# Optimization experiments

Measured on AMD Instinct MI355X. Metric: run time of the kernel, lower is better.

The kernel has to match this reference:

```python
import jax, jax.numpy as jnp
import numpy as np

INPUT_DIM = 512
DEGREE = 3
NUM_KNOTS = 16
NUM_NEURONS = 1024
OUTPUT_DIM = 512
NUM_BASIS = NUM_KNOTS + DEGREE - 1  # 18


def make_knots():
    # uniform grid on [0,1], extended by `degree` knots on each side
    h = 1.0 / (NUM_KNOTS - 1)
    grid = np.linspace(0.0, 1.0, NUM_KNOTS)
    lo = grid[0] - h * np.arange(DEGREE, 0, -1)
    hi = grid[-1] + h * np.arange(1, DEGREE + 1)
    return jnp.asarray(np.concatenate([lo, grid, hi]), dtype=jnp.float32)  # [NUM_KNOTS+2*DEGREE]


def bspline_basis(x, t, degree):
    # x: [B, N]; t: [K] uniform extended knots. Cox-de Boor recursion.
    K = t.shape[0]
    xb = x[..., None]
    B = ((xb >= t[:-1]) & (xb < t[1:])).astype(x.dtype)  # [B, N, K-1]
    for p in range(1, degree + 1):
        ti = t[: K - p - 1]
        tip = t[p : K - 1]
        ti1 = t[1 : K - p]
        tip1 = t[p + 1 : K]
        left = (xb - ti) / (tip - ti) * B[..., :-1]
        right = (tip1 - xb) / (tip1 - ti1) * B[..., 1:]
        B = left + right
    return B  # [B, N, K-1-degree] == [B, N, NUM_BASIS]


def norm_layer(x, eps=1e-8):
    # per-row min-max normalization into the spline domain [0,1)
    mn = jnp.min(x, axis=-1, keepdims=True)
    mx = jnp.max(x, axis=-1, keepdims=True)
    return (x - mn) / (mx - mn + eps)


def setup_inputs() -> dict:
    key = jax.random.key(0)
    ks = jax.random.split(key, 7)
    x = jax.random.normal(ks[0], (4096, INPUT_DIM), dtype=jnp.float32)
    s1 = 1.0 / np.sqrt(INPUT_DIM)
    s2 = 1.0 / np.sqrt(NUM_NEURONS)
    W1 = jax.random.uniform(ks[1], (INPUT_DIM, NUM_NEURONS), jnp.float32, -s1, s1)
    b1 = jax.random.uniform(ks[2], (NUM_NEURONS,), jnp.float32, -s1, s1)
    coeff = jax.random.normal(ks[3], (NUM_NEURONS, NUM_BASIS), dtype=jnp.float32) * 0.1
    sp_bias = jnp.zeros((NUM_NEURONS,), dtype=jnp.float32)
    W2 = jax.random.uniform(ks[4], (NUM_NEURONS, OUTPUT_DIM), jnp.float32, -s2, s2)
    b2 = jax.random.uniform(ks[5], (OUTPUT_DIM,), jnp.float32, -s2, s2)
    return {"x": x, "W1": W1, "b1": b1, "coeff": coeff, "sp_bias": sp_bias, "W2": W2, "b2": b2}


def reference(x, W1, b1, coeff, sp_bias, W2, b2):
    t = make_knots()
    h = x @ W1 + b1                      # [B, N]  Linear 1
    h = norm_layer(h)                    # NormLayer -> [0,1)
    basis = bspline_basis(h, t, DEGREE)  # [B, N, NUM_BASIS]
    sp = jnp.einsum('bnk,nk->bn', basis, coeff) + sp_bias  # per-neuron spline eval
    out = sp @ W2 + b2                   # Linear 2
    return jax.nn.relu(out)
```

## Files before the change

kernel.cpp:

```cpp
#include <hip/hip_runtime.h>

#define M_ROWS  4096
#define IN_DIM  512
#define NEURONS 1024
#define OUT_DIM 512

typedef _Float16 f16;
typedef __attribute__((ext_vector_type(8))) _Float16 f16x8;
typedef __attribute__((ext_vector_type(4))) _Float16 f16x4;
typedef __attribute__((ext_vector_type(4))) float    f32x4;

__global__ __launch_bounds__(256) void prep(
    const float* __restrict__ x,  f16* __restrict__ xh,
    const float* __restrict__ W1, f16* __restrict__ W1t,
    const float* __restrict__ W2, f16* __restrict__ W2t,
    const float* __restrict__ coeff, const float* __restrict__ spb,
    f16* __restrict__ cpH)
{
    __shared__ float S[32][33];
    const int b = blockIdx.x, t = threadIdx.x;
    if (b < 1024) {
        int i = b * 256 + t;
        const float4* p = (const float4*)x;
        float4 a = p[i * 2], c = p[i * 2 + 1];
        f16x8 o = { (f16)a.x, (f16)a.y, (f16)a.z, (f16)a.w,
                    (f16)c.x, (f16)c.y, (f16)c.z, (f16)c.w };
        *(f16x8*)(xh + (size_t)i * 8) = o;
        return;
    }
    if (b < 1536) {
        const int tile = b - 1024;
        const int tx = tile & 31, ty = tile >> 5;
        const int tr = t >> 3, tc = (t & 7) * 4;
        float4 v = *(const float4*)&W1[(size_t)(ty * 32 + tr) * NEURONS + tx * 32 + tc];
        S[tr][tc + 0] = v.x; S[tr][tc + 1] = v.y;
        S[tr][tc + 2] = v.z; S[tr][tc + 3] = v.w;
        __syncthreads();
        f16x4 o = {(f16)S[tc + 0][tr], (f16)S[tc + 1][tr],
                   (f16)S[tc + 2][tr], (f16)S[tc + 3][tr]};
        *(f16x4*)&W1t[(size_t)(tx * 32 + tr) * IN_DIM + ty * 32 + tc] = o;
        return;
    }
    if (b < 2048) {
        const int tile = b - 1536;
        const int nt = tile & 15, kt2 = tile >> 4;
        const int tr = t >> 3, tc = (t & 7) * 4;
        float4 v = *(const float4*)&W2[(size_t)(kt2 * 32 + tr) * OUT_DIM + nt * 32 + tc];
        S[tr][tc + 0] = v.x; S[tr][tc + 1] = v.y;
        S[tr][tc + 2] = v.z; S[tr][tc + 3] = v.w;
        __syncthreads();
        const int n = nt * 32 + tr;
        f16x4 o = {(f16)S[tc + 0][tr], (f16)S[tc + 1][tr],
                   (f16)S[tc + 2][tr], (f16)S[tc + 3][tr]};
        const int kbyte = ((kt2 * 32 + tc) * 2) ^ ((n & 7) << 4);
        *(f16x4*)((char*)W2t + (size_t)n * 2048 + kbyte) = o;
        return;
    }
    {
        const int tid = (b - 2048) * 256 + t;
        if (tid < NEURONS * 15) {
            const int n = tid / 15, ii = tid % 15;
            const float s = spb[n];
            f16x4 c;
            c[0] = (f16)(coeff[n * 18 + ii]     + s);
            c[1] = (f16)(coeff[n * 18 + ii + 1] + s);
            c[2] = (f16)(coeff[n * 18 + ii + 2] + s);
            c[3] = (f16)(coeff[n * 18 + ii + 3] + s);
            *(f16x4*)&cpH[(size_t)tid * 4] = c;
        }
    }
}

__global__ __launch_bounds__(256) void k_gemm1(
    const f16* __restrict__ A, const f16* __restrict__ Bt,
    const float* __restrict__ b1, f16* __restrict__ h,
    float* __restrict__ pmin, float* __restrict__ pmax)
{
    __shared__ f16 lds[2][(128 + 64) * 64];

    const int t    = threadIdx.x;
    const int lane = t & 63, l15 = lane & 15, lhi = lane >> 4;
    const int wid  = t >> 6;
    const int wm   = wid >> 1, wn = wid & 1;

    const int flat = blockIdx.y * gridDim.x + blockIdx.x;
    const int swz  = (flat & 7) * 64 + (flat >> 3);
    const int m0   = (swz >> 4) * 128;
    const int n0   = (swz & 15) * 64;

    auto stage = [&](int buf, int kt) {
        f16* base = &lds[buf][0];
#pragma unroll
        for (int j = 0; j < 4; ++j) {
            int c = wid * 4 + j;
            const f16* g = A + (size_t)(m0 + c * 8 + (lane >> 3)) * IN_DIM + kt + (lane & 7) * 8;
            __builtin_amdgcn_global_load_lds(
                (const __attribute__((address_space(1))) void*)g,
                (__attribute__((address_space(3))) void*)(base + c * 512), 16, 0, 0);
        }
#pragma unroll
        for (int j = 0; j < 2; ++j) {
            int c = wid * 2 + j;
            const f16* g = Bt + (size_t)(n0 + c * 8 + (lane >> 3)) * IN_DIM + kt + (lane & 7) * 8;
            __builtin_amdgcn_global_load_lds(
                (const __attribute__((address_space(1))) void*)g,
                (__attribute__((address_space(3))) void*)(base + 8192 + c * 512), 16, 0, 0);
        }
    };

    f32x4 acc[4][2];
#pragma unroll
    for (int i = 0; i < 4; ++i)
#pragma unroll
        for (int j = 0; j < 2; ++j) acc[i][j] = (f32x4)0.f;

    stage(0, 0);
    __syncthreads();

    int cur = 0;
    for (int tt = 0; tt < 8; ++tt) {
        if (tt < 7) stage(cur ^ 1, (tt + 1) * 64);
        const f16* L = &lds[cur][0];
#pragma unroll
        for (int ks = 0; ks < 2; ++ks) {
            f16x8 bfr[2];
#pragma unroll
            for (int nj = 0; nj < 2; ++nj)
                bfr[nj] = *(const f16x8*)
                    &L[8192 + (wn * 32 + nj * 16 + l15) * 64 + ks * 32 + lhi * 8];
#pragma unroll
            for (int mi = 0; mi < 4; ++mi) {
                f16x8 afr = *(const f16x8*)
                    &L[(wm * 64 + mi * 16 + l15) * 64 + ks * 32 + lhi * 8];
#pragma unroll
                for (int nj = 0; nj < 2; ++nj)
                    acc[mi][nj] = __builtin_amdgcn_mfma_f32_16x16x32_f16(
                        afr, bfr[nj], acc[mi][nj], 0, 0, 0);
            }
        }
        __syncthreads();
        cur ^= 1;
    }

    const int nb2 = (n0 >> 6) * 2 + wn;
#pragma unroll
    for (int mi = 0; mi < 4; ++mi) {
        const int row0 = m0 + wm * 64 + mi * 16 + lhi * 4;
        float vmn[4], vmx[4];
#pragma unroll
        for (int nj = 0; nj < 2; ++nj) {
            const int col = n0 + wn * 32 + nj * 16 + l15;
            const float bv = b1[col];
#pragma unroll
            for (int j = 0; j < 4; ++j) {
                f16 hv = (f16)(acc[mi][nj][j] + bv);
                h[(size_t)(row0 + j) * NEURONS + col] = hv;
                float vr = (float)hv;
                if (nj == 0) { vmn[j] = vr; vmx[j] = vr; }
                else { vmn[j] = fminf(vmn[j], vr); vmx[j] = fmaxf(vmx[j], vr); }
            }
        }
#pragma unroll
        for (int j = 0; j < 4; ++j) {
#pragma unroll
            for (int d = 1; d < 16; d <<= 1) {
                vmn[j] = fminf(vmn[j], __shfl_xor(vmn[j], d));
                vmx[j] = fmaxf(vmx[j], __shfl_xor(vmx[j], d));
            }
        }
        if (l15 == 0) {
#pragma unroll
            for (int j = 0; j < 4; ++j) {
                pmin[(size_t)nb2 * M_ROWS + row0 + j] = vmn[j];
                pmax[(size_t)nb2 * M_ROWS + row0 + j] = vmx[j];
            }
        }
    }
}

__global__ __launch_bounds__(256) void sp_gemm2(
    const f16* __restrict__ h, const float* __restrict__ pmin,
    const float* __restrict__ pmax, const f16* __restrict__ cpH,
    const f16* __restrict__ W2t, const float* __restrict__ b2,
    float* __restrict__ out)
{
    __shared__ __align__(16) f16 Bb[2][128 * 64];
    __shared__ __align__(16) f16 Aa[2][32 * 72];
    __shared__ __align__(16) f16 cpS[2][4096];
    __shared__ float mnS[32], invS[32];

    const int t    = threadIdx.x;
    const int lane = t & 63, l15 = lane & 15, lhi = lane >> 4;
    const int wid  = t >> 6;
    const int wm   = wid & 1, wn = wid >> 1;

    const int flat = blockIdx.x;
    const int swz  = (flat & 7) * 64 + (flat >> 3);
    const int m0   = (swz & 127) * 32;
    const int n0   = (swz >> 7) * 128;

    auto stageB = [&](int s) {
        f16* base = &Bb[s & 1][0];
#pragma unroll
        for (int j = 0; j < 4; ++j) {
            const int c = wid * 4 + j;
            const char* src = (const char*)W2t + (size_t)(n0 + c * 8 + (lane >> 3)) * 2048
                              + s * 128 + (lane & 7) * 16;
            __builtin_amdgcn_global_load_lds(
                (const __attribute__((address_space(1))) void*)src,
                (__attribute__((address_space(3))) void*)((char*)base + c * 1024),
                16, 0, 0);
        }
    };
    auto stageCp = [&](int s) {
        const char* src = (const char*)cpH + (size_t)s * 7680 + (wid * 64 + lane) * 16;
        char* base = (char*)&cpS[s & 1][0];
        __builtin_amdgcn_global_load_lds(
            (const __attribute__((address_space(1))) void*)src,
            (__attribute__((address_space(3))) void*)(base + wid * 1024), 16, 0, 0);
        __builtin_amdgcn_global_load_lds(
            (const __attribute__((address_space(1))) void*)(src + 4096),
            (__attribute__((address_space(3))) void*)(base + 4096 + wid * 1024), 16, 0, 0);
    };
    auto splineA = [&](int s) {
        const int r_  = t >> 3;
        const int ks8 = (t & 7) * 8;
        const int kg  = s * 64 + ks8;
        f16x8 hv = *(const f16x8*)&h[(size_t)(m0 + r_) * NEURONS + kg];
        const float mn = mnS[r_], inv = invS[r_];
        const f16* cps = &cpS[s & 1][0];
        f16x8 o;
#pragma unroll
        for (int e = 0; e < 8; ++e) {
            const float u   = ((float)hv[e] - mn) * inv;
            const float t15 = u * 15.0f;
            int ii = (int)t15;
            ii = ii < 0 ? 0 : (ii > 14 ? 14 : ii);
            const float tl  = t15 - (float)ii;
            const float t2  = tl * tl, t3 = t2 * tl;
            const float omt = 1.0f - tl;
            const float b0  = omt * omt * omt * (1.0f / 6.0f);
            const float b3v = t3 * (1.0f / 6.0f);
            const float b1v = (4.0f / 6.0f) - t2 + 0.5f * t3;
            const float b2v = (1.0f / 6.0f) + 0.5f * (tl + t2 - t3);
            const f16x4 c   = *(const f16x4*)&cps[((ks8 + e) * 15 + ii) * 4];
            o[e] = (f16)((float)c[0] * b0 + (float)c[1] * b1v
                       + (float)c[2] * b2v + (float)c[3] * b3v);
        }
        *(f16x8*)&Aa[s & 1][r_ * 72 + ks8] = o;
    };

    stageCp(0); stageCp(1); stageB(0);
    if (t < 32) {
        const int row = m0 + t;
        float a = pmin[row], b = pmax[row];
#pragma unroll
        for (int p = 1; p < 32; ++p) {
            a = fminf(a, pmin[(size_t)p * M_ROWS + row]);
            b = fmaxf(b, pmax[(size_t)p * M_ROWS + row]);
        }
        mnS[t] = a;
        invS[t] = 1.0f / (b - a + 1e-8f);
    }
    __syncthreads();
    splineA(0);
    __syncthreads();

    f32x4 acc[4];
#pragma unroll
    for (int j = 0; j < 4; ++j) acc[j] = (f32x4)0.f;

    for (int s = 0; s < 16; ++s) {
        if (s + 1 < 16) stageB(s + 1);
        if (s + 2 < 16) stageCp(s + 2);
        if (s + 1 < 16) splineA(s + 1);
        const char* B_ = (const char*)&Bb[s & 1][0];
        const f16*  A_ = &Aa[s & 1][0];
#pragma unroll
        for (int ks = 0; ks < 2; ++ks) {
            f16x8 afr = *(const f16x8*)&A_[(wm * 16 + l15) * 72 + ks * 32 + lhi * 8];
#pragma unroll
            for (int nj = 0; nj < 4; ++nj) {
                const int cl = wn * 64 + nj * 16 + l15;
                const int kb = (ks * 64 + lhi * 16) ^ ((cl & 7) << 4);
                f16x8 bfr = *(const f16x8*)(B_ + (size_t)cl * 128 + kb);
                acc[nj] = __builtin_amdgcn_mfma_f32_16x16x32_f16(afr, bfr, acc[nj], 0, 0, 0);
            }
        }
        __syncthreads();
    }

    const int row0 = m0 + wm * 16 + lhi * 4;
#pragma unroll
    for (int nj = 0; nj < 4; ++nj) {
        const int col = n0 + wn * 64 + nj * 16 + l15;
        const float bv = b2[col];
#pragma unroll
        for (int j = 0; j < 4; ++j)
            out[(size_t)(row0 + j) * OUT_DIM + col] =
                fmaxf(acc[nj][j] + bv, 0.0f);
    }
}

extern "C" void kernel_launch(void* const* d_in, const int* in_sizes, int n_in,
                              void* d_out, int out_size, void* d_ws, size_t ws_size,
                              hipStream_t stream)
{
    const float* x     = (const float*)d_in[0];
    const float* W1    = (const float*)d_in[1];
    const float* b1    = (const float*)d_in[2];
    const float* coeff = (const float*)d_in[3];
    const float* spb   = (const float*)d_in[4];
    const float* W2    = (const float*)d_in[5];
    const float* b2    = (const float*)d_in[6];
    float* out = (float*)d_out;

    char* ws = (char*)d_ws;
    f16*   h    = (f16*)ws;
    f16*   xh   = (f16*)(ws + ( 8u << 20));
    f16*   W1t  = (f16*)(ws + (12u << 20));
    f16*   W2t  = (f16*)(ws + (13u << 20));
    float* pmin = (float*)(ws + (14u << 20));
    float* pmax = (float*)(ws + (14u << 20) + (512u << 10));
    f16*   cpH  = (f16*)(ws + (15u << 20));

    prep<<<dim3(2108), 256, 0, stream>>>(x, xh, W1, W1t, W2, W2t, coeff, spb, cpH);

    k_gemm1<<<dim3(16, 32), 256, 0, stream>>>(xh, W1t, b1, h, pmin, pmax);

    sp_gemm2<<<dim3(512), 256, 0, stream>>>(h, pmin, pmax, cpH, W2t, b2, out);
}
```

Measured before the change: 47.98 us.

## Retile spline-GEMM2 to full-width 16-row blocks so spline is computed once per row

The second kernel switches from 32x128 output tiles (spline basis recomputed by each of the four column blocks) to 16x512 tiles, so each block evaluates the spline for its rows exactly once and covers all output columns. B staging now loads the full 512-column slab into a single buffer each step, with a barrier between compute and refill instead of double buffering. The per-row min/max reduction is parallelised across threads through shared memory, and h loads are prefetched two steps ahead. In exchange, the grid shrinks to 256 blocks, which is about one block per CU, and losing B double buffering can expose load latency.

```diff
diff --git a/kernel.cpp b/kernel.cpp
--- a/kernel.cpp
+++ b/kernel.cpp
@@ -184,56 +184,73 @@
     const f16* __restrict__ W2t, const float* __restrict__ b2,
     float* __restrict__ out)
 {
-    __shared__ __align__(16) f16 Bb[2][128 * 64];
-    __shared__ __align__(16) f16 Aa[2][32 * 72];
+    __shared__ __align__(16) f16 Bb[512 * 64];
+    __shared__ __align__(16) f16 Aa[2][16 * 72];
     __shared__ __align__(16) f16 cpS[2][4096];
-    __shared__ float mnS[32], invS[32];
+    __shared__ float red[2][16][17];
+    __shared__ float mnS[16], inv15S[16];
 
     const int t    = threadIdx.x;
     const int lane = t & 63, l15 = lane & 15, lhi = lane >> 4;
     const int wid  = t >> 6;
-    const int wm   = wid & 1, wn = wid >> 1;
 
     const int flat = blockIdx.x;
-    const int swz  = (flat & 7) * 64 + (flat >> 3);
-    const int m0   = (swz & 127) * 32;
-    const int n0   = (swz >> 7) * 128;
+    const int swz  = (flat & 7) * 32 + (flat >> 3);
+    const int m0   = swz * 16;
 
     auto stageB = [&](int s) {
-        f16* base = &Bb[s & 1][0];
-#pragma unroll
-        for (int j = 0; j < 4; ++j) {
-            const int c = wid * 4 + j;
-            const char* src = (const char*)W2t + (size_t)(n0 + c * 8 + (lane >> 3)) * 2048
+        char* base = (char*)&Bb[0];
+#pragma unroll
+        for (int j = 0; j < 16; ++j) {
+            const int r = wid * 128 + j * 8 + (lane >> 3);
+            const char* src = (const char*)W2t + (size_t)r * 2048
                               + s * 128 + (lane & 7) * 16;
             __builtin_amdgcn_global_load_lds(
                 (const __attribute__((address_space(1))) void*)src,
-                (__attribute__((address_space(3))) void*)((char*)base + c * 1024),
+                (__attribute__((address_space(3))) void*)(base + (size_t)r * 128
+                                                          + (lane & 7) * 16 - (size_t)(lane & 7) * 16
+                                                          + (wid * 128 + j * 8) * 128),
+                0, 0, 0);
+        }
+    };
+    (void)stageB;
+
+    auto stageB2 = [&](int s) {
+        char* base = (char*)&Bb[0];
+#pragma unroll
+        for (int j = 0; j < 16; ++j) {
+            const int rg = wid * 128 + j * 8;
+            const char* src = (const char*)W2t + (size_t)(rg + (lane >> 3)) * 2048
+                              + s * 128 + (lane & 7) * 16;
+            __builtin_amdgcn_global_load_lds(
+                (const __attribute__((address_space(1))) void*)src,
+                (__attribute__((address_space(3))) void*)(base + (size_t)rg * 128),
                 16, 0, 0);
         }
     };
     auto stageCp = [&](int s) {
-        const char* src = (const char*)cpH + (size_t)s * 7680 + (wid * 64 + lane) * 16;
+        const char* src = (const char*)cpH + (size_t)s * 7680 + t * 16;
         char* base = (char*)&cpS[s & 1][0];
         __builtin_amdgcn_global_load_lds(
-            (const __attribute__((address_space(1))) void*)src,
-            (__attribute__((address_space(3))) void*)(base + wid * 1024), 16, 0, 0);
+            (const __attribute__((address_space(1))) void*)(src),
+            (__attribute__((address_space(3))) void*)(base + (t >> 6) * 1024), 16, 0, 0);
         __builtin_amdgcn_global_load_lds(
             (const __attribute__((address_space(1))) void*)(src + 4096),
-            (__attribute__((address_space(3))) void*)(base + 4096 + wid * 1024), 16, 0, 0);
-    };
-    auto splineA = [&](int s) {
-        const int r_  = t >> 3;
-        const int ks8 = (t & 7) * 8;
-        const int kg  = s * 64 + ks8;
-        f16x8 hv = *(const f16x8*)&h[(size_t)(m0 + r_) * NEURONS + kg];
-        const float mn = mnS[r_], inv = invS[r_];
+            (__attribute__((address_space(3))) void*)(base + 4096 + (t >> 6) * 1024), 16, 0, 0);
+    };
+
+    const int sr_ = t >> 4;
+    const int skc = (t & 15) * 4;
+    auto loadH = [&](int s) -> f16x4 {
+        return *(const f16x4*)&h[(size_t)(m0 + sr_) * NEURONS + s * 64 + skc];
+    };
+    auto splineA = [&](int s, f16x4 hv) {
+        const float mn = mnS[sr_], inv15 = inv15S[sr_];
         const f16* cps = &cpS[s & 1][0];
-        f16x8 o;
-#pragma unroll
-        for (int e = 0; e < 8; ++e) {
-            const float u   = ((float)hv[e] - mn) * inv;
-            const float t15 = u * 15.0f;
+        f16x4 o;
+#pragma unroll
+        for (int e = 0; e < 4; ++e) {
+            const float t15 = ((float)hv[e] - mn) * inv15;
             int ii = (int)t15;
             ii = ii < 0 ? 0 : (ii > 14 ? 14 : ii);
             const float tl  = t15 - (float)ii;
@@ -243,57 +260,73 @@
             const float b3v = t3 * (1.0f / 6.0f);
             const float b1v = (4.0f / 6.0f) - t2 + 0.5f * t3;
             const float b2v = (1.0f / 6.0f) + 0.5f * (tl + t2 - t3);
-            const f16x4 c   = *(const f16x4*)&cps[((ks8 + e) * 15 + ii) * 4];
+            const f16x4 c   = *(const f16x4*)&cps[((skc + e) * 15 + ii) * 4];
             o[e] = (f16)((float)c[0] * b0 + (float)c[1] * b1v
                        + (float)c[2] * b2v + (float)c[3] * b3v);
         }
-        *(f16x8*)&Aa[s & 1][r_ * 72 + ks8] = o;
-    };
-
-    stageCp(0); stageCp(1); stageB(0);
-    if (t < 32) {
-        const int row = m0 + t;
-        float a = pmin[row], b = pmax[row];
-#pragma unroll
-        for (int p = 1; p < 32; ++p) {
-            a = fminf(a, pmin[(size_t)p * M_ROWS + row]);
-            b = fmaxf(b, pmax[(size_t)p * M_ROWS + row]);
+        *(f16x4*)&Aa[s & 1][sr_ * 72 + skc] = o;
+    };
+
+    stageCp(0); stageCp(1); stageB2(0);
+    {
+        const int r_ = t & 15, p = t >> 4;
+        const int row = m0 + r_;
+        red[0][r_][p] = fminf(pmin[(size_t)p * M_ROWS + row],
+                              pmin[(size_t)(p + 16) * M_ROWS + row]);
+        red[1][r_][p] = fmaxf(pmax[(size_t)p * M_ROWS + row],
+                              pmax[(size_t)(p + 16) * M_ROWS + row]);
+    }
+    __syncthreads();
+    if (t < 16) {
+        float a = red[0][t][0], b = red[1][t][0];
+#pragma unroll
+        for (int p = 1; p < 16; ++p) {
+            a = fminf(a, red[0][t][p]);
+            b = fmaxf(b, red[1][t][p]);
         }
         mnS[t] = a;
-        invS[t] = 1.0f / (b - a + 1e-8f);
-    }
+        inv15S[t] = 15.0f / (b - a + 1e-8f);
+    }
+    f16x4 hcur, hnext;
+    hcur = loadH(0);
+    hnext = loadH(1);
     __syncthreads();
-    splineA(0);
+    splineA(0, hcur);
+    hcur = hnext;
+    hnext = loadH(2);
     __syncthreads();
 
-    f32x4 acc[4];
-#pragma unroll
-    for (int j = 0; j < 4; ++j) acc[j] = (f32x4)0.f;
+    f32x4 acc[8];
+#pragma unroll
+    for (int j = 0; j < 8; ++j) acc[j] = (f32x4)0.f;
 
     for (int s = 0; s < 16; ++s) {
-        if (s + 1 < 16) stageB(s + 1);
-        if (s + 2 < 16) stageCp(s + 2);
-        if (s + 1 < 16) splineA(s + 1);
-        const char* B_ = (const char*)&Bb[s & 1][0];
-        const f16*  A_ = &Aa[s & 1][0];
 #pragma unroll
         for (int ks = 0; ks < 2; ++ks) {
-            f16x8 afr = *(const f16x8*)&A_[(wm * 16 + l15) * 72 + ks * 32 + lhi * 8];
-#pragma unroll
-            for (int nj = 0; nj < 4; ++nj) {
-                const int cl = wn * 64 + nj * 16 + l15;
+            f16x8 afr = *(const f16x8*)&Aa[s & 1][l15 * 72 + ks * 32 + lhi * 8];
+#pragma unroll
+            for (int nj = 0; nj < 8; ++nj) {
+                const int cl = wid * 128 + nj * 16 + l15;
                 const int kb = (ks * 64 + lhi * 16) ^ ((cl & 7) << 4);
-                f16x8 bfr = *(const f16x8*)(B_ + (size_t)cl * 128 + kb);
+                f16x8 bfr = *(const f16x8*)((const char*)&Bb[0] + (size_t)cl * 128 + kb);
                 acc[nj] = __builtin_amdgcn_mfma_f32_16x16x32_f16(afr, bfr, acc[nj], 0, 0, 0);
             }
         }
         __syncthreads();
-    }
-
-    const int row0 = m0 + wm * 16 + lhi * 4;
-#pragma unroll
-    for (int nj = 0; nj < 4; ++nj) {
-        const int col = n0 + wn * 64 + nj * 16 + l15;
+        if (s + 1 < 16) {
+            stageB2(s + 1);
+            if (s + 2 < 16) stageCp(s + 2);
+            splineA(s + 1, hcur);
+            hcur = hnext;
+            if (s + 3 < 16) hnext = loadH(s + 3);
+            __syncthreads();
+        }
+    }
+
+    const int row0 = m0 + lhi * 4;
+#pragma unroll
+    for (int nj = 0; nj < 8; ++nj) {
+        const int col = wid * 128 + nj * 16 + l15;
         const float bv = b2[col];
 #pragma unroll
         for (int j = 0; j < 4; ++j)
@@ -328,5 +361,5 @@
 
     k_gemm1<<<dim3(16, 32), 256, 0, stream>>>(xh, W1t, b1, h, pmin, pmax);
 
-    sp_gemm2<<<dim3(512), 256, 0, stream>>>(h, pmin, pmax, cpH, W2t, b2, out);
+    sp_gemm2<<<dim3(256), 256, 0, stream>>>(h, pmin, pmax, cpH, W2t, b2, out);
 }
```

After: 52.18 us. +8.7%, slower.

## Fuse row min-max and spline into GEMM1 with full-row tiles, plain GEMM2

Applied to the files above, without the earlier changes.

GEMM1 now computes a full 16x1024 row strip per block, so the per-row min/max normalization is reduced inside the block. The spline evaluation runs in that same epilogue and writes the spline output (sph) instead of h plus partial min/max buffers. GEMM2 becomes a plain swizzled-LDS GEMM on the precomputed spline activations, with the W1t/W2t swizzle changed to a 4-way XOR. This removes the pmin/pmax round trip and the spline work that sat inside the GEMM2 loop. In exchange GEMM1 runs on only 256 blocks with 64 KB-per-stage LDS buffers and 16 accumulators per wave, and the cpH gather now reads from global memory.

```diff
diff --git a/kernel.cpp b/kernel.cpp
--- a/kernel.cpp
+++ b/kernel.cpp
@@ -36,9 +36,11 @@
         S[tr][tc + 0] = v.x; S[tr][tc + 1] = v.y;
         S[tr][tc + 2] = v.z; S[tr][tc + 3] = v.w;
         __syncthreads();
+        const int n = tx * 32 + tr;
         f16x4 o = {(f16)S[tc + 0][tr], (f16)S[tc + 1][tr],
                    (f16)S[tc + 2][tr], (f16)S[tc + 3][tr]};
-        *(f16x4*)&W1t[(size_t)(tx * 32 + tr) * IN_DIM + ty * 32 + tc] = o;
+        const int kbyte = ((ty * 32 + tc) * 2) ^ ((n & 3) << 4);
+        *(f16x4*)((char*)W1t + (size_t)n * 1024 + kbyte) = o;
         return;
     }
     if (b < 2048) {
@@ -52,7 +54,7 @@
         const int n = nt * 32 + tr;
         f16x4 o = {(f16)S[tc + 0][tr], (f16)S[tc + 1][tr],
                    (f16)S[tc + 2][tr], (f16)S[tc + 3][tr]};
-        const int kbyte = ((kt2 * 32 + tc) * 2) ^ ((n & 7) << 4);
+        const int kbyte = ((kt2 * 32 + tc) * 2) ^ ((n & 3) << 4);
         *(f16x4*)((char*)W2t + (size_t)n * 2048 + kbyte) = o;
         return;
     }
@@ -71,169 +73,126 @@
     }
 }
 
-__global__ __launch_bounds__(256) void k_gemm1(
-    const f16* __restrict__ A, const f16* __restrict__ Bt,
-    const float* __restrict__ b1, f16* __restrict__ h,
-    float* __restrict__ pmin, float* __restrict__ pmax)
+__global__ __launch_bounds__(256) void k1_gemm1_spline(
+    const f16* __restrict__ xh, const f16* __restrict__ W1t,
+    const float* __restrict__ b1, const f16* __restrict__ cpH,
+    f16* __restrict__ sph)
 {
-    __shared__ f16 lds[2][(128 + 64) * 64];
+    __shared__ __align__(16) f16 Bb[2][1024 * 32];
 
     const int t    = threadIdx.x;
     const int lane = t & 63, l15 = lane & 15, lhi = lane >> 4;
     const int wid  = t >> 6;
-    const int wm   = wid >> 1, wn = wid & 1;
-
-    const int flat = blockIdx.y * gridDim.x + blockIdx.x;
-    const int swz  = (flat & 7) * 64 + (flat >> 3);
-    const int m0   = (swz >> 4) * 128;
-    const int n0   = (swz & 15) * 64;
-
-    auto stage = [&](int buf, int kt) {
-        f16* base = &lds[buf][0];
-#pragma unroll
-        for (int j = 0; j < 4; ++j) {
-            int c = wid * 4 + j;
-            const f16* g = A + (size_t)(m0 + c * 8 + (lane >> 3)) * IN_DIM + kt + (lane & 7) * 8;
-            __builtin_amdgcn_global_load_lds(
-                (const __attribute__((address_space(1))) void*)g,
-                (__attribute__((address_space(3))) void*)(base + c * 512), 16, 0, 0);
-        }
-#pragma unroll
-        for (int j = 0; j < 2; ++j) {
-            int c = wid * 2 + j;
-            const f16* g = Bt + (size_t)(n0 + c * 8 + (lane >> 3)) * IN_DIM + kt + (lane & 7) * 8;
-            __builtin_amdgcn_global_load_lds(
-                (const __attribute__((address_space(1))) void*)g,
-                (__attribute__((address_space(3))) void*)(base + 8192 + c * 512), 16, 0, 0);
-        }
-    };
-
-    f32x4 acc[4][2];
-#pragma unroll
-    for (int i = 0; i < 4; ++i)
-#pragma unroll
-        for (int j = 0; j < 2; ++j) acc[i][j] = (f32x4)0.f;
-
-    stage(0, 0);
-    __syncthreads();
-
-    int cur = 0;
-    for (int tt = 0; tt < 8; ++tt) {
-        if (tt < 7) stage(cur ^ 1, (tt + 1) * 64);
-        const f16* L = &lds[cur][0];
-#pragma unroll
-        for (int ks = 0; ks < 2; ++ks) {
-            f16x8 bfr[2];
-#pragma unroll
-            for (int nj = 0; nj < 2; ++nj)
-                bfr[nj] = *(const f16x8*)
-                    &L[8192 + (wn * 32 + nj * 16 + l15) * 64 + ks * 32 + lhi * 8];
-#pragma unroll
-            for (int mi = 0; mi < 4; ++mi) {
-                f16x8 afr = *(const f16x8*)
-                    &L[(wm * 64 + mi * 16 + l15) * 64 + ks * 32 + lhi * 8];
-#pragma unroll
-                for (int nj = 0; nj < 2; ++nj)
-                    acc[mi][nj] = __builtin_amdgcn_mfma_f32_16x16x32_f16(
-                        afr, bfr[nj], acc[mi][nj], 0, 0, 0);
-            }
-        }
-        __syncthreads();
-        cur ^= 1;
-    }
-
-    const int nb2 = (n0 >> 6) * 2 + wn;
-#pragma unroll
-    for (int mi = 0; mi < 4; ++mi) {
-        const int row0 = m0 + wm * 64 + mi * 16 + lhi * 4;
-        float vmn[4], vmx[4];
-#pragma unroll
-        for (int nj = 0; nj < 2; ++nj) {
-            const int col = n0 + wn * 32 + nj * 16 + l15;
-            const float bv = b1[col];
-#pragma unroll
-            for (int j = 0; j < 4; ++j) {
-                f16 hv = (f16)(acc[mi][nj][j] + bv);
-                h[(size_t)(row0 + j) * NEURONS + col] = hv;
-                float vr = (float)hv;
-                if (nj == 0) { vmn[j] = vr; vmx[j] = vr; }
-                else { vmn[j] = fminf(vmn[j], vr); vmx[j] = fmaxf(vmx[j], vr); }
-            }
-        }
-#pragma unroll
-        for (int j = 0; j < 4; ++j) {
-#pragma unroll
-            for (int d = 1; d < 16; d <<= 1) {
-                vmn[j] = fminf(vmn[j], __shfl_xor(vmn[j], d));
-                vmx[j] = fmaxf(vmx[j], __shfl_xor(vmx[j], d));
-            }
-        }
-        if (l15 == 0) {
-#pragma unroll
-            for (int j = 0; j < 4; ++j) {
-                pmin[(size_t)nb2 * M_ROWS + row0 + j] = vmn[j];
-                pmax[(size_t)nb2 * M_ROWS + row0 + j] = vmx[j];
-            }
-        }
-    }
-}
-
-__global__ __launch_bounds__(256) void sp_gemm2(
-    const f16* __restrict__ h, const float* __restrict__ pmin,
-    const float* __restrict__ pmax, const f16* __restrict__ cpH,
-    const f16* __restrict__ W2t, const float* __restrict__ b2,
-    float* __restrict__ out)
-{
-    __shared__ __align__(16) f16 Bb[2][128 * 64];
-    __shared__ __align__(16) f16 Aa[2][32 * 72];
-    __shared__ __align__(16) f16 cpS[2][4096];
-    __shared__ float mnS[32], invS[32];
-
-    const int t    = threadIdx.x;
-    const int lane = t & 63, l15 = lane & 15, lhi = lane >> 4;
-    const int wid  = t >> 6;
-    const int wm   = wid & 1, wn = wid >> 1;
 
     const int flat = blockIdx.x;
-    const int swz  = (flat & 7) * 64 + (flat >> 3);
-    const int m0   = (swz & 127) * 32;
-    const int n0   = (swz >> 7) * 128;
+    const int swz  = (flat & 7) * 32 + (flat >> 3);
+    const int m0   = swz * 16;
 
     auto stageB = [&](int s) {
-        f16* base = &Bb[s & 1][0];
-#pragma unroll
-        for (int j = 0; j < 4; ++j) {
-            const int c = wid * 4 + j;
-            const char* src = (const char*)W2t + (size_t)(n0 + c * 8 + (lane >> 3)) * 2048
-                              + s * 128 + (lane & 7) * 16;
+        char* base = (char*)&Bb[s & 1][0];
+#pragma unroll
+        for (int j = 0; j < 16; ++j) {
+            const int rg  = wid * 256 + j * 16;
+            const int row = rg + (lane >> 2);
+            const char* src = (const char*)W1t + (size_t)row * 1024
+                              + s * 64 + (lane & 3) * 16;
             __builtin_amdgcn_global_load_lds(
                 (const __attribute__((address_space(1))) void*)src,
-                (__attribute__((address_space(3))) void*)((char*)base + c * 1024),
+                (__attribute__((address_space(3))) void*)(base + rg * 64),
                 16, 0, 0);
         }
     };
-    auto stageCp = [&](int s) {
-        const char* src = (const char*)cpH + (size_t)s * 7680 + (wid * 64 + lane) * 16;
-        char* base = (char*)&cpS[s & 1][0];
-        __builtin_amdgcn_global_load_lds(
-            (const __attribute__((address_space(1))) void*)src,
-            (__attribute__((address_space(3))) void*)(base + wid * 1024), 16, 0, 0);
-        __builtin_amdgcn_global_load_lds(
-            (const __attribute__((address_space(1))) void*)(src + 4096),
-            (__attribute__((address_space(3))) void*)(base + 4096 + wid * 1024), 16, 0, 0);
+    auto loadA = [&](int s) -> f16x8 {
+        return *(const f16x8*)&xh[(size_t)(m0 + l15) * IN_DIM + s * 32 + lhi * 8];
     };
-    auto splineA = [&](int s) {
-        const int r_  = t >> 3;
-        const int ks8 = (t & 7) * 8;
-        const int kg  = s * 64 + ks8;
-        f16x8 hv = *(const f16x8*)&h[(size_t)(m0 + r_) * NEURONS + kg];
-        const float mn = mnS[r_], inv = invS[r_];
-        const f16* cps = &cpS[s & 1][0];
+
+    f32x4 acc[16];
+#pragma unroll
+    for (int j = 0; j < 16; ++j) acc[j] = (f32x4)0.f;
+
+    f16x8 aCur = loadA(0);
+    stageB(0);
+    f16x8 aNxt = loadA(1);
+    __syncthreads();
+
+    for (int s = 0; s < 16; ++s) {
+        if (s + 1 < 16) stageB(s + 1);
+        const f16x8 afr = aCur;
+        aCur = aNxt;
+        if (s + 2 < 16) aNxt = loadA(s + 2);
+        const char* B_ = (const char*)&Bb[s & 1][0];
+#pragma unroll
+        for (int nj = 0; nj < 16; ++nj) {
+            const int cl = wid * 256 + nj * 16 + l15;
+            const int kb = (lhi * 16) ^ ((cl & 3) << 4);
+            f16x8 bfr = *(const f16x8*)(B_ + (size_t)cl * 64 + kb);
+            acc[nj] = __builtin_amdgcn_mfma_f32_16x16x32_f16(afr, bfr, acc[nj], 0, 0, 0);
+        }
+        __syncthreads();
+    }
+
+    char*  ovl    = (char*)&Bb[0][0];
+    float* redmn  = (float*)ovl;
+    float* redmx  = (float*)(ovl + 256);
+    float* mnS    = (float*)(ovl + 512);
+    float* inv15S = (float*)(ovl + 576);
+    f16*   htile  = (f16*)(ovl + 1024);
+
+    float vmn[4], vmx[4];
+#pragma unroll
+    for (int nj = 0; nj < 16; ++nj) {
+        const int col = wid * 256 + nj * 16 + l15;
+        const float bv = b1[col];
+#pragma unroll
+        for (int j = 0; j < 4; ++j) {
+            f16 xv = (f16)(acc[nj][j] + bv);
+            htile[(lhi * 4 + j) * 1032 + col] = xv;
+            float vr = (float)xv;
+            if (nj == 0) { vmn[j] = vr; vmx[j] = vr; }
+            else { vmn[j] = fminf(vmn[j], vr); vmx[j] = fmaxf(vmx[j], vr); }
+        }
+    }
+#pragma unroll
+    for (int j = 0; j < 4; ++j) {
+#pragma unroll
+        for (int d = 1; d < 16; d <<= 1) {
+            vmn[j] = fminf(vmn[j], __shfl_xor(vmn[j], d));
+            vmx[j] = fmaxf(vmx[j], __shfl_xor(vmx[j], d));
+        }
+    }
+    if (l15 == 0) {
+#pragma unroll
+        for (int j = 0; j < 4; ++j) {
+            redmn[wid * 16 + lhi * 4 + j] = vmn[j];
+            redmx[wid * 16 + lhi * 4 + j] = vmx[j];
+        }
+    }
+    __syncthreads();
+    if (t < 16) {
+        float a = redmn[t], bb = redmx[t];
+#pragma unroll
+        for (int w = 1; w < 4; ++w) {
+            a  = fminf(a,  redmn[w * 16 + t]);
+            bb = fmaxf(bb, redmx[w * 16 + t]);
+        }
+        mnS[t]    = a;
+        inv15S[t] = 15.0f / (bb - a + 1e-8f);
+    }
+    __syncthreads();
+
+    const int r_  = t >> 4;
+    const int c0q = (t & 15) * 64;
+    const float mn = mnS[r_], inv15 = inv15S[r_];
+    const int grow = m0 + r_;
+    const int sK   = (grow & 3) << 4;
+#pragma unroll
+    for (int q = 0; q < 8; ++q) {
+        f16x8 hvv = *(const f16x8*)&htile[r_ * 1032 + c0q + q * 8];
         f16x8 o;
 #pragma unroll
         for (int e = 0; e < 8; ++e) {
-            const float u   = ((float)hv[e] - mn) * inv;
-            const float t15 = u * 15.0f;
+            const int n = c0q + q * 8 + e;
+            const float t15 = ((float)hvv[e] - mn) * inv15;
             int ii = (int)t15;
             ii = ii < 0 ? 0 : (ii > 14 ? 14 : ii);
             const float tl  = t15 - (float)ii;
@@ -243,62 +202,100 @@
             const float b3v = t3 * (1.0f / 6.0f);
             const float b1v = (4.0f / 6.0f) - t2 + 0.5f * t3;
             const float b2v = (1.0f / 6.0f) + 0.5f * (tl + t2 - t3);
-            const f16x4 c   = *(const f16x4*)&cps[((ks8 + e) * 15 + ii) * 4];
+            const f16x4 c   = *(const f16x4*)&cpH[((size_t)n * 15 + ii) * 4];
             o[e] = (f16)((float)c[0] * b0 + (float)c[1] * b1v
                        + (float)c[2] * b2v + (float)c[3] * b3v);
         }
-        *(f16x8*)&Aa[s & 1][r_ * 72 + ks8] = o;
+        const int kbyte = ((c0q + q * 8) * 2) ^ sK;
+        *(f16x8*)((char*)sph + (size_t)grow * 2048 + kbyte) = o;
+    }
+}
+
+__global__ __launch_bounds__(256) void k_gemm2(
+    const f16* __restrict__ A, const f16* __restrict__ Bt,
+    const float* __restrict__ b2, float* __restrict__ out)
+{
+    __shared__ f16 lds[2][128 * 128];
+
+    const int t    = threadIdx.x;
+    const int lane = t & 63, l15 = lane & 15, lhi = lane >> 4;
+    const int wid  = t >> 6;
+    const int wm   = wid >> 1, wn = wid & 1;
+
+    const int flat = blockIdx.x;
+    const int swz  = (flat & 7) * 64 + (flat >> 3);
+    const int m0   = (swz >> 3) * 64;
+    const int n0   = (swz & 7) * 64;
+
+    auto stage = [&](int buf, int kt) {
+        f16* base = &lds[buf][0];
+#pragma unroll
+        for (int j = 0; j < 4; ++j) {
+            int c = wid * 4 + j;
+            const f16* g = A + (size_t)(m0 + c * 4 + (lane >> 4)) * NEURONS + kt + (lane & 15) * 8;
+            __builtin_amdgcn_global_load_lds(
+                (const __attribute__((address_space(1))) void*)g,
+                (__attribute__((address_space(3))) void*)(base + c * 512), 16, 0, 0);
+        }
+#pragma unroll
+        for (int j = 0; j < 4; ++j) {
+            int c = wid * 4 + j;
+            const f16* g = Bt + (size_t)(n0 + c * 4 + (lane >> 4)) * NEURONS + kt + (lane & 15) * 8;
+            __builtin_amdgcn_global_load_lds(
+                (const __attribute__((address_space(1))) void*)g,
+                (__attribute__((address_space(3))) void*)(base + 8192 + c * 512), 16, 0, 0);
+        }
     };
 
-    stageCp(0); stageCp(1); stageB(0);
-    if (t < 32) {
-        const int row = m0 + t;
-        float a = pmin[row], b = pmax[row];
-#pragma unroll
-        for (int p = 1; p < 32; ++p) {
-            a = fminf(a, pmin[(size_t)p * M_ROWS + row]);
-            b = fmaxf(b, pmax[(size_t)p * M_ROWS + row]);
-        }
-        mnS[t] = a;
-        invS[t] = 1.0f / (b - a + 1e-8f);
-    }
+    f32x4 acc[2][2];
+#pragma unroll
+    for (int i = 0; i < 2; ++i)
+#pragma unroll
+        for (int j = 0; j < 2; ++j) acc[i][j] = (f32x4)0.f;
+
+    stage(0, 0);
     __syncthreads();
-    splineA(0);
-    __syncthreads();
-
-    f32x4 acc[4];
-#pragma unroll
-    for (int j = 0; j < 4; ++j) acc[j] = (f32x4)0.f;
-
-    for (int s = 0; s < 16; ++s) {
-        if (s + 1 < 16) stageB(s + 1);
-        if (s + 2 < 16) stageCp(s + 2);
-        if (s + 1 < 16) splineA(s + 1);
-        const char* B_ = (const char*)&Bb[s & 1][0];
-        const f16*  A_ = &Aa[s & 1][0];
-#pragma unroll
-        for (int ks = 0; ks < 2; ++ks) {
-            f16x8 afr = *(const f16x8*)&A_[(wm * 16 + l15) * 72 + ks * 32 + lhi * 8];
-#pragma unroll
-            for (int nj = 0; nj < 4; ++nj) {
-                const int cl = wn * 64 + nj * 16 + l15;
-                const int kb = (ks * 64 + lhi * 16) ^ ((cl & 7) << 4);
-                f16x8 bfr = *(const f16x8*)(B_ + (size_t)cl * 128 + kb);
-                acc[nj] = __builtin_amdgcn_mfma_f32_16x16x32_f16(afr, bfr, acc[nj], 0, 0, 0);
+
+    const int sA = (l15 & 3) << 4;
+    int cur = 0;
+    for (int tt = 0; tt < 8; ++tt) {
+        if (tt < 7) stage(cur ^ 1, (tt + 1) * 128);
+        const char* L = (const char*)&lds[cur][0];
+#pragma unroll
+        for (int ks = 0; ks < 4; ++ks) {
+            const int ko = (ks * 64 + lhi * 16) ^ sA;
+            f16x8 bfr[2];
+#pragma unroll
+            for (int nj = 0; nj < 2; ++nj) {
+                const int cl = wn * 32 + nj * 16 + l15;
+                bfr[nj] = *(const f16x8*)(L + 16384 + (size_t)cl * 256 + ko);
             }
+#pragma unroll
+            for (int mi = 0; mi < 2; ++mi) {
+                const int ar = wm * 32 + mi * 16 + l15;
+                f16x8 afr = *(const f16x8*)(L + (size_t)ar * 256 + ko);
+#pragma unroll
+                for (int nj = 0; nj < 2; ++nj)
+                    acc[mi][nj] = __builtin_amdgcn_mfma_f32_16x16x32_f16(
+                        afr, bfr[nj], acc[mi][nj], 0, 0, 0);
+            }
         }
         __syncthreads();
-    }
-
-    const int row0 = m0 + wm * 16 + lhi * 4;
-#pragma unroll
-    for (int nj = 0; nj < 4; ++nj) {
-        const int col = n0 + wn * 64 + nj * 16 + l15;
-        const float bv = b2[col];
-#pragma unroll
-        for (int j = 0; j < 4; ++j)
-            out[(size_t)(row0 + j) * OUT_DIM + col] =
-                fmaxf(acc[nj][j] + bv, 0.0f);
+        cur ^= 1;
+    }
+
+#pragma unroll
+    for (int mi = 0; mi < 2; ++mi) {
+        const int row0 = m0 + wm * 32 + mi * 16 + lhi * 4;
+#pragma unroll
+        for (int nj = 0; nj < 2; ++nj) {
+            const int col = n0 + wn * 32 + nj * 16 + l15;
+            const float bv = b2[col];
+#pragma unroll
+            for (int j = 0; j < 4; ++j)
+                out[(size_t)(row0 + j) * OUT_DIM + col] =
+                    fmaxf(acc[mi][nj][j] + bv, 0.0f);
+        }
     }
 }
 
@@ -316,17 +313,15 @@
     float* out = (float*)d_out;
 
     char* ws = (char*)d_ws;
-    f16*   h    = (f16*)ws;
+    f16*   sph  = (f16*)ws;
     f16*   xh   = (f16*)(ws + ( 8u << 20));
     f16*   W1t  = (f16*)(ws + (12u << 20));
     f16*   W2t  = (f16*)(ws + (13u << 20));
-    float* pmin = (float*)(ws + (14u << 20));
-    float* pmax = (float*)(ws + (14u << 20) + (512u << 10));
-    f16*   cpH  = (f16*)(ws + (15u << 20));
+    f16*   cpH  = (f16*)(ws + (14u << 20));
 
     prep<<<dim3(2108), 256, 0, stream>>>(x, xh, W1, W1t, W2, W2t, coeff, spb, cpH);
 
-    k_gemm1<<<dim3(16, 32), 256, 0, stream>>>(xh, W1t, b1, h, pmin, pmax);
-
-    sp_gemm2<<<dim3(512), 256, 0, stream>>>(h, pmin, pmax, cpH, W2t, b2, out);
+    k1_gemm1_spline<<<dim3(256), 256, 0, stream>>>(xh, W1t, b1, cpH, sph);
+
+    k_gemm2<<<dim3(512), 256, 0, stream>>>(sph, W2t, b2, out);
 }
```

After: 55.92 us. +16.5%, slower.

## Prefetch h tiles into LDS asynchronously and use fine-grained vmcnt waits in sp_gemm2

Applied to the files above, without the earlier changes.

The spline+GEMM2 kernel now stages the h activation tile into a double-buffered LDS area with async global-to-LDS loads two steps ahead, in place of a direct global load inside the spline evaluation. The loop's __syncthreads calls become explicit lgkmcnt waits plus raw barriers, with partial vmcnt counts so that only the loads needed for the next stage are awaited and later prefetches stay in flight. This is meant to hide the global latency of h behind the MFMA work. In exchange it uses more LDS and relies on hand-counted vmcnt values, which can race if the count of outstanding loads is wrong.

```diff
diff --git a/kernel.cpp b/kernel.cpp
--- a/kernel.cpp
+++ b/kernel.cpp
@@ -9,6 +9,10 @@
 typedef __attribute__((ext_vector_type(8))) _Float16 f16x8;
 typedef __attribute__((ext_vector_type(4))) _Float16 f16x4;
 typedef __attribute__((ext_vector_type(4))) float    f32x4;
+
+#define GLD(srcp, dstp) __builtin_amdgcn_global_load_lds( \
+    (const __attribute__((address_space(1))) void*)(srcp), \
+    (__attribute__((address_space(3))) void*)(dstp), 16, 0, 0)
 
 __global__ __launch_bounds__(256) void prep(
     const float* __restrict__ x,  f16* __restrict__ xh,
@@ -93,18 +97,14 @@
 #pragma unroll
         for (int j = 0; j < 4; ++j) {
             int c = wid * 4 + j;
-            const f16* g = A + (size_t)(m0 + c * 8 + (lane >> 3)) * IN_DIM + kt + (lane & 7) * 8;
-            __builtin_amdgcn_global_load_lds(
-                (const __attribute__((address_space(1))) void*)g,
-                (__attribute__((address_space(3))) void*)(base + c * 512), 16, 0, 0);
+            GLD(A + (size_t)(m0 + c * 8 + (lane >> 3)) * IN_DIM + kt + (lane & 7) * 8,
+                base + c * 512);
         }
 #pragma unroll
         for (int j = 0; j < 2; ++j) {
             int c = wid * 2 + j;
-            const f16* g = Bt + (size_t)(n0 + c * 8 + (lane >> 3)) * IN_DIM + kt + (lane & 7) * 8;
-            __builtin_amdgcn_global_load_lds(
-                (const __attribute__((address_space(1))) void*)g,
-                (__attribute__((address_space(3))) void*)(base + 8192 + c * 512), 16, 0, 0);
+            GLD(Bt + (size_t)(n0 + c * 8 + (lane >> 3)) * IN_DIM + kt + (lane & 7) * 8,
+                base + 8192 + c * 512);
         }
     };
 
@@ -187,6 +187,7 @@
     __shared__ __align__(16) f16 Bb[2][128 * 64];
     __shared__ __align__(16) f16 Aa[2][32 * 72];
     __shared__ __align__(16) f16 cpS[2][4096];
+    __shared__ __align__(16) f16 hS[2][32 * 64];
     __shared__ float mnS[32], invS[32];
 
     const int t    = threadIdx.x;
@@ -200,35 +201,32 @@
     const int n0   = (swz >> 7) * 128;
 
     auto stageB = [&](int s) {
-        f16* base = &Bb[s & 1][0];
+        char* base = (char*)&Bb[s & 1][0];
 #pragma unroll
         for (int j = 0; j < 4; ++j) {
             const int c = wid * 4 + j;
-            const char* src = (const char*)W2t + (size_t)(n0 + c * 8 + (lane >> 3)) * 2048
-                              + s * 128 + (lane & 7) * 16;
-            __builtin_amdgcn_global_load_lds(
-                (const __attribute__((address_space(1))) void*)src,
-                (__attribute__((address_space(3))) void*)((char*)base + c * 1024),
-                16, 0, 0);
+            GLD((const char*)W2t + (size_t)(n0 + c * 8 + (lane >> 3)) * 2048
+                    + s * 128 + (lane & 7) * 16,
+                base + c * 1024);
         }
     };
     auto stageCp = [&](int s) {
         const char* src = (const char*)cpH + (size_t)s * 7680 + (wid * 64 + lane) * 16;
         char* base = (char*)&cpS[s & 1][0];
-        __builtin_amdgcn_global_load_lds(
-            (const __attribute__((address_space(1))) void*)src,
-            (__attribute__((address_space(3))) void*)(base + wid * 1024), 16, 0, 0);
-        __builtin_amdgcn_global_load_lds(
-            (const __attribute__((address_space(1))) void*)(src + 4096),
-            (__attribute__((address_space(3))) void*)(base + 4096 + wid * 1024), 16, 0, 0);
-    };
+        GLD(src,        base + wid * 1024);
+        GLD(src + 4096, base + 4096 + wid * 1024);
+    };
+    auto stageH = [&](int s) {
+        GLD(h + (size_t)(m0 + wid * 8 + (lane >> 3)) * NEURONS + s * 64 + (lane & 7) * 8,
+            (char*)&hS[s & 1][0] + wid * 1024);
+    };
+
+    const int sr_ = t >> 3;
+    const int sk8 = (t & 7) * 8;
     auto splineA = [&](int s) {
-        const int r_  = t >> 3;
-        const int ks8 = (t & 7) * 8;
-        const int kg  = s * 64 + ks8;
-        f16x8 hv = *(const f16x8*)&h[(size_t)(m0 + r_) * NEURONS + kg];
-        const float mn = mnS[r_], inv = invS[r_];
+        const float mn = mnS[sr_], inv = invS[sr_];
         const f16* cps = &cpS[s & 1][0];
+        f16x8 hv = *(const f16x8*)&hS[s & 1][sr_ * 64 + sk8];
         f16x8 o;
 #pragma unroll
         for (int e = 0; e < 8; ++e) {
@@ -243,14 +241,14 @@
             const float b3v = t3 * (1.0f / 6.0f);
             const float b1v = (4.0f / 6.0f) - t2 + 0.5f * t3;
             const float b2v = (1.0f / 6.0f) + 0.5f * (tl + t2 - t3);
-            const f16x4 c   = *(const f16x4*)&cps[((ks8 + e) * 15 + ii) * 4];
+            const f16x4 c   = *(const f16x4*)&cps[((sk8 + e) * 15 + ii) * 4];
             o[e] = (f16)((float)c[0] * b0 + (float)c[1] * b1v
                        + (float)c[2] * b2v + (float)c[3] * b3v);
         }
-        *(f16x8*)&Aa[s & 1][r_ * 72 + ks8] = o;
-    };
-
-    stageCp(0); stageCp(1); stageB(0);
+        *(f16x8*)&Aa[s & 1][sr_ * 72 + sk8] = o;
+    };
+
+    stageB(0); stageCp(0); stageCp(1); stageH(0); stageH(1);
     if (t < 32) {
         const int row = m0 + t;
         float a = pmin[row], b = pmax[row];
@@ -264,7 +262,9 @@
     }
     __syncthreads();
     splineA(0);
-    __syncthreads();
+    asm volatile("s_waitcnt lgkmcnt(0)" ::: "memory");
+    __builtin_amdgcn_s_barrier();
+    __builtin_amdgcn_sched_barrier(0);
 
     f32x4 acc[4];
 #pragma unroll
@@ -272,22 +272,30 @@
 
     for (int s = 0; s < 16; ++s) {
         if (s + 1 < 16) stageB(s + 1);
-        if (s + 2 < 16) stageCp(s + 2);
+        if (s + 2 < 16) { stageCp(s + 2); stageH(s + 2); }
+        if (s + 2 < 16)      { asm volatile("s_waitcnt vmcnt(7)" ::: "memory"); }
+        else if (s + 1 < 16) { asm volatile("s_waitcnt vmcnt(4)" ::: "memory"); }
+        else                 { asm volatile("s_waitcnt vmcnt(0)" ::: "memory"); }
+        __builtin_amdgcn_sched_barrier(0);
         if (s + 1 < 16) splineA(s + 1);
-        const char* B_ = (const char*)&Bb[s & 1][0];
-        const f16*  A_ = &Aa[s & 1][0];
-#pragma unroll
-        for (int ks = 0; ks < 2; ++ks) {
-            f16x8 afr = *(const f16x8*)&A_[(wm * 16 + l15) * 72 + ks * 32 + lhi * 8];
-#pragma unroll
-            for (int nj = 0; nj < 4; ++nj) {
-                const int cl = wn * 64 + nj * 16 + l15;
-                const int kb = (ks * 64 + lhi * 16) ^ ((cl & 7) << 4);
-                f16x8 bfr = *(const f16x8*)(B_ + (size_t)cl * 128 + kb);
-                acc[nj] = __builtin_amdgcn_mfma_f32_16x16x32_f16(afr, bfr, acc[nj], 0, 0, 0);
-            }
-        }
-        __syncthreads();
+        {
+            const char* B_ = (const char*)&Bb[s & 1][0];
+            const f16*  A_ = &Aa[s & 1][0];
+#pragma unroll
+            for (int ks = 0; ks < 2; ++ks) {
+                f16x8 afr = *(const f16x8*)&A_[(wm * 16 + l15) * 72 + ks * 32 + lhi * 8];
+#pragma unroll
+                for (int nj = 0; nj < 4; ++nj) {
+                    const int cl = wn * 64 + nj * 16 + l15;
+                    const int kb = (ks * 64 + lhi * 16) ^ ((cl & 7) << 4);
+                    f16x8 bfr = *(const f16x8*)(B_ + (size_t)cl * 128 + kb);
+                    acc[nj] = __builtin_amdgcn_mfma_f32_16x16x32_f16(afr, bfr, acc[nj], 0, 0, 0);
+                }
+            }
+        }
+        asm volatile("s_waitcnt lgkmcnt(0)" ::: "memory");
+        __builtin_amdgcn_s_barrier();
+        __builtin_amdgcn_sched_barrier(0);
     }
 
     const int row0 = m0 + wm * 16 + lhi * 4;
```

Result: slower. 49.29 us (+2.7%).
